# Kernel optimization log

Hardware: AMD Instinct MI355X
Metric: run time of the kernel (lower is better)

Reference implementation:

```python
import jax, jax.numpy as jnp
import numpy as np

B = 8192
N_MELS = 80
AUX = 32
RNN = 512
FC = 512
N_CLASSES = 512


def gru_cell(x, h, w_ih, w_hh, b_ih, b_hh):
    # torch.nn.GRUCell semantics; w_* are [3*H, in], gates ordered (r, z, n)
    gi = x @ w_ih.T + b_ih
    gh = h @ w_hh.T + b_hh
    i_r, i_z, i_n = jnp.split(gi, 3, axis=1)
    h_r, h_z, h_n = jnp.split(gh, 3, axis=1)
    r = jax.nn.sigmoid(i_r + h_r)
    z = jax.nn.sigmoid(i_z + h_z)
    n = jnp.tanh(i_n + r * h_n)
    return (1.0 - z) * n + z * h


def setup_inputs() -> dict:
    key = jax.random.key(0)
    ks = jax.random.split(key, 32)
    s = lambda k, shp, sc=0.05: (jax.random.normal(k, shp, dtype=jnp.float32) * sc)
    inp = {
        'm_t': jax.random.normal(ks[0], (B, N_MELS), dtype=jnp.float32),
        'a1_t': jax.random.normal(ks[1], (B, AUX), dtype=jnp.float32),
        'a2_t': jax.random.normal(ks[2], (B, AUX), dtype=jnp.float32),
        'a3_t': jax.random.normal(ks[3], (B, AUX), dtype=jnp.float32),
        'a4_t': jax.random.normal(ks[4], (B, AUX), dtype=jnp.float32),
        'h1': jax.random.normal(ks[5], (B, RNN), dtype=jnp.float32),
        'h2': jax.random.normal(ks[6], (B, RNN), dtype=jnp.float32),
        'x': jax.random.normal(ks[7], (B, 1), dtype=jnp.float32),
        # params
        'I_w': s(ks[8], (RNN, 1 + N_MELS + AUX)),
        'I_b': s(ks[9], (RNN,)),
        'rnn1_wih': s(ks[10], (3 * RNN, RNN)),
        'rnn1_whh': s(ks[11], (3 * RNN, RNN)),
        'rnn1_bih': s(ks[12], (3 * RNN,)),
        'rnn1_bhh': s(ks[13], (3 * RNN,)),
        'rnn2_wih': s(ks[14], (3 * RNN, RNN + AUX)),
        'rnn2_whh': s(ks[15], (3 * RNN, RNN)),
        'rnn2_bih': s(ks[16], (3 * RNN,)),
        'rnn2_bhh': s(ks[17], (3 * RNN,)),
        'fc1_w': s(ks[18], (FC, RNN + AUX)),
        'fc1_b': s(ks[19], (FC,)),
        'fc2_w': s(ks[20], (FC, FC + AUX)),
        'fc2_b': s(ks[21], (FC,)),
        'fc3_w': s(ks[22], (N_CLASSES, FC)),
        'fc3_b': s(ks[23], (N_CLASSES,)),
    }
    return inp


def reference(m_t, a1_t, a2_t, a3_t, a4_t, h1, h2, x,
              I_w, I_b, rnn1_wih, rnn1_whh, rnn1_bih, rnn1_bhh,
              rnn2_wih, rnn2_whh, rnn2_bih, rnn2_bhh,
              fc1_w, fc1_b, fc2_w, fc2_b, fc3_w, fc3_b):
    x = jnp.concatenate([x, m_t, a1_t], axis=1)
    x = x @ I_w.T + I_b
    h1n = gru_cell(x, h1, rnn1_wih, rnn1_whh, rnn1_bih, rnn1_bhh)
    x = x + h1n
    inp = jnp.concatenate([x, a2_t], axis=1)
    h2n = gru_cell(inp, h2, rnn2_wih, rnn2_whh, rnn2_bih, rnn2_bhh)
    x = x + h2n
    x = jnp.concatenate([x, a3_t], axis=1)
    x = jax.nn.relu(x @ fc1_w.T + fc1_b)
    x = jnp.concatenate([x, a4_t], axis=1)
    x = jax.nn.relu(x @ fc2_w.T + fc2_b)
    logits = x @ fc3_w.T + fc3_b
    return (logits, h1n, h2n)
```

## Files before the change

kernel.cpp:

```cpp
#include <hip/hip_runtime.h>


#define BK 32

typedef __attribute__((ext_vector_type(8))) short short8;
typedef __attribute__((ext_vector_type(4))) float f32x4;
typedef __attribute__((ext_vector_type(8))) unsigned short ush8;

__device__ __forceinline__ unsigned short f2bf(float f) {
    unsigned int u = __float_as_uint(f);
    u += 0x7fffu + ((u >> 16) & 1u);
    return (unsigned short)(u >> 16);
}
__device__ __forceinline__ float bf2f(unsigned short h) {
    return __uint_as_float(((unsigned int)h) << 16);
}
__device__ __forceinline__ float sigm(float x)  { return 1.f / (1.f + __expf(-x)); }
__device__ __forceinline__ float tanh_f(float x){ return 1.f - 2.f / (__expf(2.f * x) + 1.f); }

__device__ __forceinline__ void gl16(const void* g, void* l) {
    __builtin_amdgcn_global_load_lds(
        (const __attribute__((address_space(1))) unsigned int*)g,
        (__attribute__((address_space(3))) unsigned int*)l, 16, 0, 0);
}

struct GruArgs {
    const float* hprev;
    const float* xprev;
    float* hn_out;
    float* x_f32_out;
    unsigned short* x_bf_out;
    int out_stride;
};

__global__ __launch_bounds__(512)
void gru_k(const unsigned short* __restrict__ A1, const unsigned short* __restrict__ A2,
           const unsigned short* __restrict__ Wih, const unsigned short* __restrict__ Whh,
           const float* __restrict__ bih, const float* __restrict__ bhh,
           int kpad, GruArgs g)
{
    extern __shared__ __align__(16) unsigned short lds[];
    constexpr int BUFU = 20480;
    const int t    = threadIdx.x;
    const int w    = t >> 6;
    const int lane = t & 63;
    const int isgi = (w < 4);
    const int ww   = w & 3;
    const int mh   = ww >> 1;
    const int nh   = ww & 1;
    const int m0   = blockIdx.x * 128;
    const int n0   = blockIdx.y * 64;
    const int fr   = lane & 15;
    const int kg   = (lane >> 4) * 8;
    const int NT   = kpad >> 5;

    f32x4 acc[3][4][2] = {};

    auto stage = [&](int buf, int k0) {
        unsigned short* dst = lds + buf * BUFU;
        #pragma unroll
        for (int k = 0; k < 5; ++k) {
            const int u = k * 512 + w * 64 + lane;
            const unsigned short* src;
            if (u < 512) {
                src = A1 + (size_t)(m0 + (u >> 2)) * kpad + k0 + (u & 3) * 8;
            } else if (u < 1024) {
                src = A2 + (size_t)(m0 + ((u - 512) >> 2)) * kpad + k0 + (u & 3) * 8;
            } else {
                const int v = u - 1024;
                const int p = v >> 8;
                const int r = (v & 255) >> 2;
                const unsigned short* Wp = (p < 3) ? Wih : Whh;
                const int s = (p < 3) ? p : p - 3;
                src = Wp + (size_t)(s * 512 + n0 + r) * kpad + k0 + (u & 3) * 8;
            }
            gl16(src, dst + (size_t)(k * 512 + w * 64) * 8);
        }
    };

    stage(0, 0);
    __syncthreads();
    int cur = 0;
    for (int tt = 0; tt < NT; ++tt) {
        if (tt + 1 < NT) stage(cur ^ 1, (tt + 1) * BK);
        const unsigned short* B0 = lds + cur * BUFU;
        const unsigned short* Ab = B0 + (isgi ? 0 : 4096);
        short8 a[4];
        #pragma unroll
        for (int mi = 0; mi < 4; ++mi)
            a[mi] = *(const short8*)(Ab + (mh * 64 + mi * 16 + fr) * 32 + kg);
        #pragma unroll
        for (int s = 0; s < 3; ++s) {
            const unsigned short* Bp = B0 + 8192 + (isgi ? s : s + 3) * 2048;
            #pragma unroll
            for (int ni = 0; ni < 2; ++ni) {
                short8 b = *(const short8*)(Bp + (nh * 32 + ni * 16 + fr) * 32 + kg);
                #pragma unroll
                for (int mi = 0; mi < 4; ++mi)
                    acc[s][mi][ni] = __builtin_amdgcn_mfma_f32_16x16x32_bf16(a[mi], b, acc[s][mi][ni], 0, 0, 0);
            }
        }
        __syncthreads();
        cur ^= 1;
    }

    float* xf = (float*)lds;
    if (!isgi) {
        #pragma unroll
        for (int s = 0; s < 2; ++s)
        #pragma unroll
        for (int mi = 0; mi < 4; ++mi)
        #pragma unroll
        for (int ni = 0; ni < 2; ++ni)
            *(f32x4*)(xf + s * 8192 + ww * 2048 + (mi * 2 + ni) * 256 + lane * 4) = acc[s][mi][ni];
    }
    __syncthreads();
    if (isgi) {
        #pragma unroll
        for (int mi = 0; mi < 4; ++mi)
        #pragma unroll
        for (int ni = 0; ni < 2; ++ni) {
            const int nn = n0 + nh * 32 + ni * 16 + fr;
            const float bir = bih[nn] + bhh[nn];
            const float biz = bih[512 + nn] + bhh[512 + nn];
            f32x4 ghr = *(const f32x4*)(xf + ww * 2048 + (mi * 2 + ni) * 256 + lane * 4);
            f32x4 ghz = *(const f32x4*)(xf + 8192 + ww * 2048 + (mi * 2 + ni) * 256 + lane * 4);
            #pragma unroll
            for (int v = 0; v < 4; ++v) {
                acc[0][mi][ni][v] = sigm(acc[0][mi][ni][v] + ghr[v] + bir);
                acc[1][mi][ni][v] = sigm(acc[1][mi][ni][v] + ghz[v] + biz);
            }
        }
    }
    __syncthreads();
    if (!isgi) {
        #pragma unroll
        for (int mi = 0; mi < 4; ++mi)
        #pragma unroll
        for (int ni = 0; ni < 2; ++ni)
            *(f32x4*)(xf + ww * 2048 + (mi * 2 + ni) * 256 + lane * 4) = acc[2][mi][ni];
    }
    __syncthreads();
    if (isgi) {
        #pragma unroll
        for (int mi = 0; mi < 4; ++mi)
        #pragma unroll
        for (int ni = 0; ni < 2; ++ni) {
            const int nn = n0 + nh * 32 + ni * 16 + fr;
            const float bin_ = bih[1024 + nn];
            const float bhn  = bhh[1024 + nn];
            f32x4 ghn = *(const f32x4*)(xf + ww * 2048 + (mi * 2 + ni) * 256 + lane * 4);
            #pragma unroll
            for (int v = 0; v < 4; ++v) {
                const int m = m0 + mh * 64 + mi * 16 + (lane >> 4) * 4 + v;
                const size_t r0 = (size_t)m * 512;
                float r  = acc[0][mi][ni][v];
                float z  = acc[1][mi][ni][v];
                float nv = tanh_f(acc[2][mi][ni][v] + bin_ + r * (ghn[v] + bhn));
                float h  = g.hprev[r0 + nn];
                float hv = (1.f - z) * nv + z * h;
                g.hn_out[r0 + nn] = hv;
                float xv = g.xprev[r0 + nn] + hv;
                if (g.x_f32_out) g.x_f32_out[r0 + nn] = xv;
                g.x_bf_out[(size_t)m * g.out_stride + nn] = f2bf(xv);
            }
        }
    }
}

struct EpiArgs { float* f32_out; unsigned short* bf_h; int out_stride; };

template<int EPI>
__global__ __launch_bounds__(256)
void gemm_k(const unsigned short* __restrict__ A, const unsigned short* __restrict__ W,
            const float* __restrict__ bias, int kpad, EpiArgs ea)
{
    constexpr int BUFU = 8 * 512;
    __shared__ __align__(16) unsigned short lds[2 * BUFU];
    const int t    = threadIdx.x;
    const int m0   = blockIdx.x * 64;
    const int n0   = blockIdx.y * 64;
    const int lane = t & 63;
    const int w    = t >> 6;
    const int rl   = lane >> 2;
    const int cl   = (lane & 3) * 8;
    const int fr   = lane & 15;
    const int kg   = (lane >> 4) * 8;

    f32x4 acc[4] = {};
    const int NT = kpad >> 5;

    auto stage = [&](int buf, int k0) {
        unsigned short* dst = lds + buf * BUFU;
        gl16(A + (size_t)(m0 + w * 16 + rl) * kpad + (k0 + cl), dst + w * 512);
        gl16(W + (size_t)(n0 + w * 16 + rl) * kpad + (k0 + cl), dst + (4 + w) * 512);
    };

    stage(0, 0);
    __syncthreads();
    int cur = 0;
    for (int tt = 0; tt < NT; ++tt) {
        if (tt + 1 < NT) stage(cur ^ 1, (tt + 1) * BK);
        const unsigned short* Bb = lds + cur * BUFU;
        short8 b = *(const short8*)(Bb + 2048 + (w * 16 + fr) * 32 + kg);
        #pragma unroll
        for (int mi = 0; mi < 4; ++mi) {
            short8 a = *(const short8*)(Bb + (mi * 16 + fr) * 32 + kg);
            acc[mi] = __builtin_amdgcn_mfma_f32_16x16x32_bf16(a, b, acc[mi], 0, 0, 0);
        }
        __syncthreads();
        cur ^= 1;
    }

    const int nn = n0 + w * 16 + fr;
    const float bv = bias[nn];
    #pragma unroll
    for (int mi = 0; mi < 4; ++mi)
    #pragma unroll
    for (int v = 0; v < 4; ++v) {
        const int m = m0 + mi * 16 + (lane >> 4) * 4 + v;
        float val = acc[mi][v] + bv;
        if constexpr (EPI == 0) {
            const size_t o = (size_t)m * 512 + nn;
            ea.f32_out[o] = val;
            ea.bf_h[o] = f2bf(val);
        } else if constexpr (EPI == 3) {
            val = fmaxf(val, 0.f);
            ea.bf_h[(size_t)m * ea.out_stride + nn] = f2bf(val);
        } else {
            ea.f32_out[(size_t)m * 512 + nn] = val;
        }
    }
}

struct SplitSeg { const float* src; unsigned short* dh; int K; int Kpad; int total; };
struct SplitArgs { SplitSeg seg[10]; };

__global__ void k_split(SplitArgs a) {
    const SplitSeg s = a.seg[blockIdx.y];
    const int stride = gridDim.x * blockDim.x;
    const int tid0 = blockIdx.x * blockDim.x + threadIdx.x;
    if (s.K == s.Kpad) {
        const int n8 = s.total >> 3;
        const float4* src4 = (const float4*)s.src;
        ush8* dst8 = (ush8*)s.dh;
        for (int i = tid0; i < n8; i += stride) {
            float4 f0 = src4[i * 2];
            float4 f1 = src4[i * 2 + 1];
            ush8 o;
            o[0] = f2bf(f0.x); o[1] = f2bf(f0.y); o[2] = f2bf(f0.z); o[3] = f2bf(f0.w);
            o[4] = f2bf(f1.x); o[5] = f2bf(f1.y); o[6] = f2bf(f1.z); o[7] = f2bf(f1.w);
            dst8[i] = o;
        }
    } else {
        for (int i = tid0; i < s.total; i += stride) {
            int row = i / s.Kpad;
            int col = i - row * s.Kpad;
            float v = (col < s.K) ? s.src[(size_t)row * s.K + col] : 0.f;
            s.dh[i] = f2bf(v);
        }
    }
}

__global__ void k_build_c0(const float* __restrict__ x, const float* __restrict__ m,
                           const float* __restrict__ a1, unsigned short* __restrict__ dh) {
    int i = blockIdx.x * blockDim.x + threadIdx.x;
    int row = i >> 7, col = i & 127;
    float v = 0.f;
    if (col == 0)       v = x[row];
    else if (col < 81)  v = m[row * 80 + (col - 1)];
    else if (col < 113) v = a1[row * 32 + (col - 81)];
    dh[i] = f2bf(v);
}

__global__ void k_fill_tail(unsigned short* __restrict__ dh, const float* __restrict__ src) {
    int i = blockIdx.x * blockDim.x + threadIdx.x;
    int row = i >> 6, col = i & 63;
    float v = (col < 32) ? src[row * 32 + col] : 0.f;
    dh[(size_t)row * 576 + 512 + col] = f2bf(v);
}

extern "C" void kernel_launch(void* const* d_in, const int* in_sizes, int n_in,
                              void* d_out, int out_size, void* d_ws, size_t ws_size,
                              hipStream_t stream)
{
    const size_t OFF_WI   = 0;
    const size_t OFF_W1IH = 131072;
    const size_t OFF_W1HH = 1703936;
    const size_t OFF_W2IH = 3276800;
    const size_t OFF_W2HH = 5046272;
    const size_t OFF_WFC1 = 6815744;
    const size_t OFF_WFC2 = 7405568;
    const size_t OFF_WFC3 = 7995392;
    const size_t OFF_H1   = 8519680;
    const size_t OFF_H2   = 16908288;
    const size_t OFF_C0   = 26345472;
    const size_t OFF_X0H  = 28442624;
    const size_t OFF_X0F  = 36831232;
    const size_t OFF_X1F  = 53608448;
    const size_t OFF_X1C  = 70385664;
    const size_t OFF_X2C  = 79822848;
    const size_t OFF_X3C  = 89260032;
    const size_t OFF_X4   = 98697216;
    const size_t WS_NEEDED = 107085824;
    if (ws_size < WS_NEEDED) return;

    const float* m_t   = (const float*)d_in[0];
    const float* a1    = (const float*)d_in[1];
    const float* a2    = (const float*)d_in[2];
    const float* a3    = (const float*)d_in[3];
    const float* a4    = (const float*)d_in[4];
    const float* h1    = (const float*)d_in[5];
    const float* h2    = (const float*)d_in[6];
    const float* xin   = (const float*)d_in[7];
    const float* I_w   = (const float*)d_in[8];
    const float* I_b   = (const float*)d_in[9];
    const float* r1wih = (const float*)d_in[10];
    const float* r1whh = (const float*)d_in[11];
    const float* r1bih = (const float*)d_in[12];
    const float* r1bhh = (const float*)d_in[13];
    const float* r2wih = (const float*)d_in[14];
    const float* r2whh = (const float*)d_in[15];
    const float* r2bih = (const float*)d_in[16];
    const float* r2bhh = (const float*)d_in[17];
    const float* fc1w  = (const float*)d_in[18];
    const float* fc1b  = (const float*)d_in[19];
    const float* fc2w  = (const float*)d_in[20];
    const float* fc2b  = (const float*)d_in[21];
    const float* fc3w  = (const float*)d_in[22];
    const float* fc3b  = (const float*)d_in[23];
    float* out = (float*)d_out;

    char* ws = (char*)d_ws;
    auto U  = [&](size_t off) { return (unsigned short*)(ws + off); };
    auto Fp = [&](size_t off) { return (float*)(ws + off); };
    (void)in_sizes; (void)n_in; (void)out_size;

    SplitArgs sa;
    sa.seg[0] = { I_w,   U(OFF_WI),   113, 128, 512 * 128 };
    sa.seg[1] = { r1wih, U(OFF_W1IH), 512, 512, 1536 * 512 };
    sa.seg[2] = { r1whh, U(OFF_W1HH), 512, 512, 1536 * 512 };
    sa.seg[3] = { r2wih, U(OFF_W2IH), 544, 576, 1536 * 576 };
    sa.seg[4] = { r2whh, U(OFF_W2HH), 512, 576, 1536 * 576 };
    sa.seg[5] = { fc1w,  U(OFF_WFC1), 544, 576, 512 * 576 };
    sa.seg[6] = { fc2w,  U(OFF_WFC2), 544, 576, 512 * 576 };
    sa.seg[7] = { fc3w,  U(OFF_WFC3), 512, 512, 512 * 512 };
    sa.seg[8] = { h1,    U(OFF_H1),   512, 512, 8192 * 512 };
    sa.seg[9] = { h2,    U(OFF_H2),   512, 576, 8192 * 576 };
    hipLaunchKernelGGL(k_split, dim3(512, 10), dim3(256), 0, stream, sa);

    hipLaunchKernelGGL(k_build_c0, dim3(4096), dim3(256), 0, stream, xin, m_t, a1, U(OFF_C0));
    hipLaunchKernelGGL(k_fill_tail, dim3(2048), dim3(256), 0, stream, U(OFF_X1C), a2);
    hipLaunchKernelGGL(k_fill_tail, dim3(2048), dim3(256), 0, stream, U(OFF_X2C), a3);
    hipLaunchKernelGGL(k_fill_tail, dim3(2048), dim3(256), 0, stream, U(OFF_X3C), a4);

    EpiArgs ea{};
    ea.f32_out = Fp(OFF_X0F); ea.bf_h = U(OFF_X0H); ea.out_stride = 512;
    hipLaunchKernelGGL((gemm_k<0>), dim3(128, 8), dim3(256), 0, stream,
                       U(OFF_C0), U(OFF_WI), I_b, 128, ea);

    GruArgs g{};
    g.hprev = h1; g.xprev = Fp(OFF_X0F);
    g.hn_out = out + 4194304; g.x_f32_out = Fp(OFF_X1F);
    g.x_bf_out = U(OFF_X1C); g.out_stride = 576;
    hipLaunchKernelGGL(gru_k, dim3(64, 8), dim3(512), 81920, stream,
                       U(OFF_X0H), U(OFF_H1), U(OFF_W1IH), U(OFF_W1HH), r1bih, r1bhh, 512, g);

    g = GruArgs{};
    g.hprev = h2; g.xprev = Fp(OFF_X1F);
    g.hn_out = out + 8388608; g.x_f32_out = nullptr;
    g.x_bf_out = U(OFF_X2C); g.out_stride = 576;
    hipLaunchKernelGGL(gru_k, dim3(64, 8), dim3(512), 81920, stream,
                       U(OFF_X1C), U(OFF_H2), U(OFF_W2IH), U(OFF_W2HH), r2bih, r2bhh, 576, g);

    ea = EpiArgs{}; ea.bf_h = U(OFF_X3C); ea.out_stride = 576;
    hipLaunchKernelGGL((gemm_k<3>), dim3(128, 8), dim3(256), 0, stream,
                       U(OFF_X2C), U(OFF_WFC1), fc1b, 576, ea);
    ea = EpiArgs{}; ea.bf_h = U(OFF_X4); ea.out_stride = 512;
    hipLaunchKernelGGL((gemm_k<3>), dim3(128, 8), dim3(256), 0, stream,
                       U(OFF_X3C), U(OFF_WFC2), fc2b, 576, ea);
    ea = EpiArgs{}; ea.f32_out = out;
    hipLaunchKernelGGL((gemm_k<4>), dim3(128, 8), dim3(256), 0, stream,
                       U(OFF_X4), U(OFF_WFC3), fc3b, 512, ea);
}
```

Baseline: 326.7 us.

## Triple-buffer GRU kernel LDS pipeline and vectorize padded split conversion

```diff
diff --git a/kernel.cpp b/kernel.cpp
--- a/kernel.cpp
+++ b/kernel.cpp
@@ -79,10 +79,16 @@
     };
 
     stage(0, 0);
-    __syncthreads();
+    stage(1, BK);
+    __builtin_amdgcn_sched_barrier(0);
+    asm volatile("s_waitcnt vmcnt(5)" ::: "memory");
+    __builtin_amdgcn_s_barrier();
+    __builtin_amdgcn_sched_barrier(0);
+
     int cur = 0;
     for (int tt = 0; tt < NT; ++tt) {
-        if (tt + 1 < NT) stage(cur ^ 1, (tt + 1) * BK);
+        const int nxt2 = (cur + 2 >= 3) ? cur - 1 : cur + 2;
+        if (tt + 2 < NT) stage(nxt2, (tt + 2) * BK);
         const unsigned short* B0 = lds + cur * BUFU;
         const unsigned short* Ab = B0 + (isgi ? 0 : 4096);
         short8 a[4];
@@ -100,8 +106,12 @@
                     acc[s][mi][ni] = __builtin_amdgcn_mfma_f32_16x16x32_bf16(a[mi], b, acc[s][mi][ni], 0, 0, 0);
             }
         }
-        __syncthreads();
-        cur ^= 1;
+        __builtin_amdgcn_sched_barrier(0);
+        if (tt + 2 < NT) asm volatile("s_waitcnt vmcnt(5)" ::: "memory");
+        else             asm volatile("s_waitcnt vmcnt(0)" ::: "memory");
+        __builtin_amdgcn_s_barrier();
+        __builtin_amdgcn_sched_barrier(0);
+        cur = (cur + 1 >= 3) ? 0 : cur + 1;
     }
 
     float* xf = (float*)lds;
@@ -240,16 +250,24 @@
     const SplitSeg s = a.seg[blockIdx.y];
     const int stride = gridDim.x * blockDim.x;
     const int tid0 = blockIdx.x * blockDim.x + threadIdx.x;
-    if (s.K == s.Kpad) {
+    if ((s.K & 7) == 0) {
         const int n8 = s.total >> 3;
-        const float4* src4 = (const float4*)s.src;
+        const int kp8 = s.Kpad >> 3;
+        const int k8  = s.K >> 3;
         ush8* dst8 = (ush8*)s.dh;
         for (int i = tid0; i < n8; i += stride) {
-            float4 f0 = src4[i * 2];
-            float4 f1 = src4[i * 2 + 1];
             ush8 o;
-            o[0] = f2bf(f0.x); o[1] = f2bf(f0.y); o[2] = f2bf(f0.z); o[3] = f2bf(f0.w);
-            o[4] = f2bf(f1.x); o[5] = f2bf(f1.y); o[6] = f2bf(f1.z); o[7] = f2bf(f1.w);
+            int row = i / kp8;
+            int c8  = i - row * kp8;
+            if (c8 < k8) {
+                const float4* src4 = (const float4*)(s.src + (size_t)row * s.K + c8 * 8);
+                float4 f0 = src4[0];
+                float4 f1 = src4[1];
+                o[0] = f2bf(f0.x); o[1] = f2bf(f0.y); o[2] = f2bf(f0.z); o[3] = f2bf(f0.w);
+                o[4] = f2bf(f1.x); o[5] = f2bf(f1.y); o[6] = f2bf(f1.z); o[7] = f2bf(f1.w);
+            } else {
+                o = ush8{0, 0, 0, 0, 0, 0, 0, 0};
+            }
             dst8[i] = o;
         }
     } else {
@@ -363,14 +381,14 @@
     g.hprev = h1; g.xprev = Fp(OFF_X0F);
     g.hn_out = out + 4194304; g.x_f32_out = Fp(OFF_X1F);
     g.x_bf_out = U(OFF_X1C); g.out_stride = 576;
-    hipLaunchKernelGGL(gru_k, dim3(64, 8), dim3(512), 81920, stream,
+    hipLaunchKernelGGL(gru_k, dim3(64, 8), dim3(512), 122880, stream,
                        U(OFF_X0H), U(OFF_H1), U(OFF_W1IH), U(OFF_W1HH), r1bih, r1bhh, 512, g);
 
     g = GruArgs{};
     g.hprev = h2; g.xprev = Fp(OFF_X1F);
     g.hn_out = out + 8388608; g.x_f32_out = nullptr;
     g.x_bf_out = U(OFF_X2C); g.out_stride = 576;
-    hipLaunchKernelGGL(gru_k, dim3(64, 8), dim3(512), 81920, stream,
+    hipLaunchKernelGGL(gru_k, dim3(64, 8), dim3(512), 122880, stream,
                        U(OFF_X1C), U(OFF_H2), U(OFF_W2IH), U(OFF_W2HH), r2bih, r2bhh, 576, g);
 
     ea = EpiArgs{}; ea.bf_h = U(OFF_X3C); ea.out_stride = 576;
```

Result: no change. 327.4 us (+0.2%).
